# Performance work log

Measured on AMD Instinct MI355X. Metric: run time of the kernel, lower is better.

## Reference

```python
import jax, jax.numpy as jnp
import numpy as np

N_HEADS = 16


def layernorm(x, g, b, eps=1e-5):
    mu = jnp.mean(x, axis=-1, keepdims=True)
    var = jnp.var(x, axis=-1, keepdims=True)
    return (x - mu) * jax.lax.rsqrt(var + eps) * g + b


def mha(x, w_qkv, b_qkv, w_o, b_o, n_heads):
    # standard multi-head self-attention (dropout off / eval mode)
    B, S, D = x.shape
    hd = D // n_heads
    qkv = x @ w_qkv + b_qkv                      # [B,S,3D]
    q, k, v = jnp.split(qkv, 3, axis=-1)
    q = q.reshape(B, S, n_heads, hd).transpose(0, 2, 1, 3)  # bhsd
    k = k.reshape(B, S, n_heads, hd).transpose(0, 2, 1, 3)
    v = v.reshape(B, S, n_heads, hd).transpose(0, 2, 1, 3)
    att = jnp.einsum('bhqd,bhkd->bhqk', q, k) / jnp.sqrt(jnp.asarray(hd, x.dtype))
    att = jax.nn.softmax(att, axis=-1)
    out = jnp.einsum('bhqk,bhkd->bhqd', att, v)
    out = out.transpose(0, 2, 1, 3).reshape(B, S, D)
    return out @ w_o + b_o


def setup_inputs() -> dict:
    key = jax.random.key(0)
    ks = jax.random.split(key, 12)
    B, Sx, Sz, D = 4, 1024, 1024, 1024
    H = D * 4
    s = 0.02
    return {
        'x': jax.random.normal(ks[0], (B, Sx, D), jnp.float32),
        'z': jax.random.normal(ks[1], (B, Sz, D), jnp.float32),
        'g1': jnp.ones((D,), jnp.float32),
        'b1': jnp.zeros((D,), jnp.float32),
        'w_qkv': jax.random.normal(ks[2], (D, 3 * D), jnp.float32) * s,
        'b_qkv': jnp.zeros((3 * D,), jnp.float32),
        'w_o': jax.random.normal(ks[3], (D, D), jnp.float32) * s,
        'b_o': jnp.zeros((D,), jnp.float32),
        'w_kv': jax.random.normal(ks[4], (D, 2 * D), jnp.float32) * s,
        'b_kv': jnp.zeros((2 * D,), jnp.float32),
        'g2': jnp.ones((D,), jnp.float32),
        'b2': jnp.zeros((D,), jnp.float32),
        'w_m1': jax.random.normal(ks[5], (D, H), jnp.float32) * s,
        'b_m1': jnp.zeros((H,), jnp.float32),
        'w_m2': jax.random.normal(ks[6], (H, D), jnp.float32) * s,
        'b_m2': jnp.zeros((D,), jnp.float32),
    }


def reference(x, z, g1, b1, w_qkv, b_qkv, w_o, b_o, w_kv, b_kv, g2, b2, w_m1, b_m1, w_m2, b_m2):
    # q = x + self_mha(ln1(x))
    q = x + mha(layernorm(x, g1, b1), w_qkv, b_qkv, w_o, b_o, N_HEADS)
    # single-head cross attention: k,v from z, scale by sqrt(dim)
    kv = z @ w_kv + b_kv
    k, v = jnp.split(kv, 2, axis=-1)            # each [B,Sz,D]
    scale = jnp.sqrt(jnp.asarray(k.shape[-1], x.dtype))
    att = jax.nn.softmax(jnp.einsum('bqd,bkd->bqk', q, k) / scale, axis=-1)
    out = jnp.einsum('bqk,bkd->bqd', att, v)
    # out = out + mlp(ln2(out))
    h = layernorm(out, g2, b2)
    h = jax.nn.gelu(h @ w_m1 + b_m1) @ w_m2 + b_m2
    return out + h
```

## Files before the change

kernel.cpp:

```cpp
#include <hip/hip_runtime.h>
#include <cstdint>
#include <cstddef>

using u16 = unsigned short;

typedef __attribute__((ext_vector_type(4))) float f32x4;
typedef __attribute__((ext_vector_type(8))) short bf16x8;

#define DEV static __device__ __forceinline__

DEV float bf2f(u16 v) {
  union { unsigned u; float f; } x; x.u = ((unsigned)v) << 16; return x.f;
}
DEV u16 f2bf(float f) {
  union { float f; unsigned u; } x; x.f = f;
  unsigned r = x.u + 0x7fffu + ((x.u >> 16) & 1u);
  return (u16)(r >> 16);
}
DEV void gload16(const void* g, void* l) {
  __builtin_amdgcn_global_load_lds((const __attribute__((address_space(1))) void*)g,
                                   (__attribute__((address_space(3))) void*)l, 16, 0, 0);
}
DEV float fast_gelu(float x) {
  const float y = 0.7978845608028654f * (x + 0.044715f * x * x * x);
  const float e = __builtin_amdgcn_exp2f(y * 2.8853900817779268f);
  const float t = 1.0f - 2.0f * __builtin_amdgcn_rcpf(e + 1.0f);
  return 0.5f * x * (1.0f + t);
}

DEV float rowmax16_dpp(float v) {
  union { float f; int i; } a, b;
  a.f = v;
  b.i = __builtin_amdgcn_update_dpp(0, a.i, 0x121, 0xf, 0xf, true); a.f = fmaxf(a.f, b.f);
  b.i = __builtin_amdgcn_update_dpp(0, a.i, 0x122, 0xf, 0xf, true); a.f = fmaxf(a.f, b.f);
  b.i = __builtin_amdgcn_update_dpp(0, a.i, 0x124, 0xf, 0xf, true); a.f = fmaxf(a.f, b.f);
  b.i = __builtin_amdgcn_update_dpp(0, a.i, 0x128, 0xf, 0xf, true); a.f = fmaxf(a.f, b.f);
  return a.f;
}

template <typename OutT, bool GELU, int BN, bool SPLIT>
__global__ __launch_bounds__(256, 4) void gemm_nt(
    const u16* __restrict__ A, const u16* __restrict__ Bt, OutT* __restrict__ C,
    int K, int lda, int ldb, int ldc,
    const float* __restrict__ bias,
    const float* __restrict__ resF, const u16* __restrict__ resB, int ldr,
    float scale,
    long long sA, long long sB, long long sC, long long sR,
    int kSlices)
{
  constexpr int NW = (BN == 128) ? 64 : 32;
  constexpr int NJ = NW / 16;
  __shared__ u16 As[128 * 32];
  __shared__ u16 Bs[BN * 32];

  const int z = blockIdx.z;
  const int bz = z / kSlices;
  const int ks = z - bz * kSlices;
  const int Ksl = K / kSlices;
  const int kbeg = ks * Ksl, kend = kbeg + Ksl;

  A  += (size_t)bz * sA;
  Bt += (size_t)bz * sB;
  if constexpr (SPLIT) C += (size_t)ks * sC;
  else                 C += (size_t)bz * sC;
  const int m0 = blockIdx.y * 128, n0 = blockIdx.x * BN;
  const int tid = threadIdx.x;
  const int lane = tid & 63, wave = tid >> 6;
  const int wm = (wave >> 1) * 64, wn = (wave & 1) * NW;
  const int m15 = lane & 15, quad = lane >> 4;

  const u16* Ab = A + (size_t)m0 * lda;
  const u16* Bb = Bt + (size_t)n0 * ldb;
  const int r0 = tid >> 2, cc8 = (tid & 3) * 8;

  f32x4 acc[4][NJ];
#pragma unroll
  for (int i = 0; i < 4; i++)
#pragma unroll
    for (int j = 0; j < NJ; j++) acc[i][j] = (f32x4){0.f, 0.f, 0.f, 0.f};

  for (int k0 = kbeg; k0 < kend; k0 += 32) {
    __syncthreads();
    gload16(Ab + (size_t)r0 * lda + k0 + cc8,        &As[tid * 8]);
    gload16(Ab + (size_t)(r0 + 64) * lda + k0 + cc8, &As[2048 + tid * 8]);
    gload16(Bb + (size_t)r0 * ldb + k0 + cc8,        &Bs[tid * 8]);
    if constexpr (BN == 128)
      gload16(Bb + (size_t)(r0 + 64) * ldb + k0 + cc8, &Bs[2048 + tid * 8]);
    __syncthreads();
    bf16x8 af[4], bfr[NJ];
#pragma unroll
    for (int i = 0; i < 4; i++) af[i]  = *(const bf16x8*)&As[(wm + i * 16 + m15) * 32 + quad * 8];
#pragma unroll
    for (int j = 0; j < NJ; j++) bfr[j] = *(const bf16x8*)&Bs[(wn + j * 16 + m15) * 32 + quad * 8];
#pragma unroll
    for (int i = 0; i < 4; i++)
#pragma unroll
      for (int j = 0; j < NJ; j++)
        acc[i][j] = __builtin_amdgcn_mfma_f32_16x16x32_bf16(af[i], bfr[j], acc[i][j], 0, 0, 0);
  }

  const float* resFb = resF ? resF + (size_t)bz * sR : nullptr;
  const u16*   resBb = resB ? resB + (size_t)bz * sR : nullptr;

#pragma unroll
  for (int i = 0; i < 4; i++) {
    const int rowb = m0 + wm + i * 16 + quad * 4;
#pragma unroll
    for (int r = 0; r < 4; r++) {
      const size_t rowoff = (size_t)(rowb + r) * ldc;
      const size_t resoff = (size_t)(rowb + r) * ldr;
#pragma unroll
      for (int j = 0; j < NJ; j++) {
        const int col = n0 + wn + j * 16 + m15;
        float v = acc[i][j][r] * scale;
        if constexpr (SPLIT) {
          ((u16*)C)[rowoff + col] = f2bf(v);
        } else {
          if (bias) v += bias[col];
          if (GELU) v = fast_gelu(v);
          if (resFb) v += resFb[resoff + col];
          if (resBb) v += bf2f(resBb[resoff + col]);
          if constexpr (sizeof(OutT) == 4) C[rowoff + col] = v;
          else ((u16*)C)[rowoff + col] = f2bf(v);
        }
      }
    }
  }
}

__global__ __launch_bounds__(256) void mlp2_reduce_k(
    const u16* __restrict__ part, long long sliceStride,
    const u16* __restrict__ outb, const float* __restrict__ b_m2,
    float* __restrict__ outF)
{
  const size_t i = (size_t)blockIdx.x * 256 + threadIdx.x;
  const int col = (int)((i * 4) & 1023);
  const ushort4 u = ((const ushort4*)outb)[i];
  float4 o;
  o.x = bf2f(u.x) + b_m2[col + 0];
  o.y = bf2f(u.y) + b_m2[col + 1];
  o.z = bf2f(u.z) + b_m2[col + 2];
  o.w = bf2f(u.w) + b_m2[col + 3];
#pragma unroll
  for (int ks = 0; ks < 4; ks++) {
    const ushort4 p = ((const ushort4*)(part + (size_t)ks * sliceStride))[i];
    o.x += bf2f(p.x); o.y += bf2f(p.y); o.z += bf2f(p.z); o.w += bf2f(p.w);
  }
  ((float4*)outF)[i] = o;
}

__global__ __launch_bounds__(256) void transpose_all_k(
    const float* __restrict__ w_qkv, const float* __restrict__ w_o,
    const float* __restrict__ w_kv,  const float* __restrict__ w_m1,
    const float* __restrict__ w_m2,
    u16* __restrict__ wqkvT, u16* __restrict__ woT, u16* __restrict__ wkvT,
    u16* __restrict__ wm1T,  u16* __restrict__ wm2T)
{
  __shared__ u16 tile[32][33];
  int idx = blockIdx.x;
  const float* in; u16* out; int gx, ldin, ldout;
  if (idx < 3072)      { in = w_qkv; out = wqkvT; gx = 96;  ldin = 3072; ldout = 1024; }
  else if (idx < 4096) { idx -= 3072; in = w_o;  out = woT;  gx = 32;  ldin = 1024; ldout = 1024; }
  else if (idx < 6144) { idx -= 4096; in = w_kv; out = wkvT; gx = 64;  ldin = 2048; ldout = 1024; }
  else if (idx < 10240){ idx -= 6144; in = w_m1; out = wm1T; gx = 128; ldin = 4096; ldout = 1024; }
  else                 { idx -= 10240; in = w_m2; out = wm2T; gx = 32; ldin = 1024; ldout = 4096; }
  const int bx = idx % gx, by = idx / gx;
  const int tx = threadIdx.x & 31, ty = threadIdx.x >> 5;
  const int x = bx * 32 + tx;
#pragma unroll
  for (int j = 0; j < 4; j++)
    tile[ty + j * 8][tx] = f2bf(in[(size_t)(by * 32 + ty + j * 8) * ldin + x]);
  __syncthreads();
  const int x2 = by * 32 + tx;
#pragma unroll
  for (int j = 0; j < 4; j++)
    out[(size_t)(bx * 32 + ty + j * 8) * ldout + x2] = tile[tx][ty + j * 8];
}

__global__ __launch_bounds__(256) void prep_k(
    const float* __restrict__ x, const float* __restrict__ g, const float* __restrict__ bb,
    u16* __restrict__ xln, const float* __restrict__ z, u16* __restrict__ zb)
{
  const int row = blockIdx.x;
  const int t = threadIdx.x;
  if (blockIdx.y == 1) {
    const size_t i = (size_t)row * 256 + t;
    const float4 f = ((const float4*)z)[i];
    ushort4 o; o.x = f2bf(f.x); o.y = f2bf(f.y); o.z = f2bf(f.z); o.w = f2bf(f.w);
    ((ushort4*)zb)[i] = o;
    return;
  }
  float v[4];
  const float4 f = ((const float4*)(x + (size_t)row * 1024))[t];
  v[0] = f.x; v[1] = f.y; v[2] = f.z; v[3] = f.w;
  float s = v[0] + v[1] + v[2] + v[3];
  float sq = v[0]*v[0] + v[1]*v[1] + v[2]*v[2] + v[3]*v[3];
#pragma unroll
  for (int off = 1; off < 64; off <<= 1) { s += __shfl_xor(s, off); sq += __shfl_xor(sq, off); }
  __shared__ float red[8];
  const int wv = t >> 6;
  if ((t & 63) == 0) { red[wv] = s; red[4 + wv] = sq; }
  __syncthreads();
  s = red[0] + red[1] + red[2] + red[3];
  sq = red[4] + red[5] + red[6] + red[7];
  const float mean = s * (1.0f / 1024.0f);
  const float var = sq * (1.0f / 1024.0f) - mean * mean;
  const float rstd = rsqrtf(var + 1e-5f);
  const int c = t * 4;
  ushort4 o;
  o.x = f2bf((v[0] - mean) * rstd * g[c + 0] + bb[c + 0]);
  o.y = f2bf((v[1] - mean) * rstd * g[c + 1] + bb[c + 1]);
  o.z = f2bf((v[2] - mean) * rstd * g[c + 2] + bb[c + 2]);
  o.w = f2bf((v[3] - mean) * rstd * g[c + 3] + bb[c + 3]);
  ((ushort4*)(xln + (size_t)row * 1024))[t] = o;
}

__global__ __launch_bounds__(256) void transpose_v_self(
    const u16* __restrict__ qkv, u16* __restrict__ vT)
{
  __shared__ u16 tile[32][33];
  const int z = blockIdx.z, b = z >> 4, h = z & 15;
  const u16* in = qkv + (size_t)b * 1024 * 3072 + 2048 + h * 64;
  u16* out = vT + (size_t)z * 64 * 1024;
  const int tx = threadIdx.x & 31, ty = threadIdx.x >> 5;
  const int key0 = blockIdx.x * 32, d0 = blockIdx.y * 32;
#pragma unroll
  for (int j = 0; j < 4; j++)
    tile[ty + j * 8][tx] = in[(size_t)(key0 + ty + j * 8) * 3072 + d0 + tx];
  __syncthreads();
#pragma unroll
  for (int j = 0; j < 4; j++)
    out[(size_t)(d0 + ty + j * 8) * 1024 + key0 + tx] = tile[tx][ty + j * 8];
}

__global__ __launch_bounds__(256, 5) void flash_self_attn3(
    const u16* __restrict__ qkv, const u16* __restrict__ vT, u16* __restrict__ outp)
{
  __shared__ u16 Ks[64 * 72];
  __shared__ u16 Vs[64 * 72];
  __shared__ u16 Ps[4][16 * 72];
  const int b = blockIdx.z, h = blockIdx.y, q0 = blockIdx.x * 64;
  const int tid = threadIdx.x;
  const int lane = tid & 63, w = tid >> 6;
  const int m15 = lane & 15, quad = lane >> 4;
  const float L2E = 1.4426950408889634f;

  const size_t base = (size_t)b * 1024 * 3072;
  const u16* qb  = qkv + base + (size_t)q0 * 3072 + h * 64;
  const u16* kb  = qkv + base + 1024 + h * 64;
  const u16* vtb = vT + (size_t)(b * 16 + h) * 64 * 1024;

  const int r8 = tid >> 3, c8 = (tid & 7) * 8;

  bf16x8 aq[2];
#pragma unroll
  for (int kk = 0; kk < 2; kk++) {
    const bf16x8 raw = *(const bf16x8*)(qb + (size_t)(w * 16 + m15) * 3072 + kk * 32 + quad * 8);
#pragma unroll
    for (int j = 0; j < 8; j++)
      ((u16*)&aq[kk])[j] = f2bf(bf2f(((const u16*)&raw)[j]) * 0.125f);
  }

  const short oneb = (short)0x3F80;
  const bf16x8 ones = {oneb, oneb, oneb, oneb, oneb, oneb, oneb, oneb};

  float mL[4];
  f32x4 lacc;
  f32x4 oacc[4];
#pragma unroll
  for (int r = 0; r < 4; r++) mL[r] = -3.0e38f;
  lacc = (f32x4){0.f, 0.f, 0.f, 0.f};
#pragma unroll
  for (int d = 0; d < 4; d++) oacc[d] = (f32x4){0.f, 0.f, 0.f, 0.f};

  for (int kt = 0; kt < 16; kt++) {
    const int key0 = kt * 64;
    bf16x8 kreg[2], vreg[2];
#pragma unroll
    for (int i = 0; i < 2; i++) {
      kreg[i] = *(const bf16x8*)(kb + (size_t)(key0 + r8 + i * 32) * 3072 + c8);
      vreg[i] = *(const bf16x8*)(vtb + (size_t)(r8 + i * 32) * 1024 + key0 + c8);
    }
    __syncthreads();
#pragma unroll
    for (int i = 0; i < 2; i++) {
      *(bf16x8*)&Ks[(r8 + i * 32) * 72 + c8] = kreg[i];
      *(bf16x8*)&Vs[(r8 + i * 32) * 72 + c8] = vreg[i];
    }
    __syncthreads();

    f32x4 sacc[4];
#pragma unroll
    for (int n = 0; n < 4; n++) sacc[n] = (f32x4){0.f, 0.f, 0.f, 0.f};
#pragma unroll
    for (int kk = 0; kk < 2; kk++)
#pragma unroll
      for (int n = 0; n < 4; n++) {
        const bf16x8 bk = *(const bf16x8*)&Ks[(n * 16 + m15) * 72 + kk * 32 + quad * 8];
        sacc[n] = __builtin_amdgcn_mfma_f32_16x16x32_bf16(aq[kk], bk, sacc[n], 0, 0, 0);
      }

    float al[4];
#pragma unroll
    for (int r = 0; r < 4; r++) {
      float v = fmaxf(fmaxf(sacc[0][r], sacc[1][r]), fmaxf(sacc[2][r], sacc[3][r]));
      v = rowmax16_dpp(v) * L2E;
      const float mnew = fmaxf(mL[r], v);
      al[r] = __builtin_amdgcn_exp2f(mL[r] - mnew);
      mL[r] = mnew;
    }
#pragma unroll
    for (int n = 0; n < 4; n++)
#pragma unroll
      for (int r = 0; r < 4; r++) {
        const float p = __builtin_amdgcn_exp2f(fmaf(sacc[n][r], L2E, -mL[r]));
        Ps[w][(quad * 4 + r) * 72 + n * 16 + m15] = f2bf(p);
      }
#pragma unroll
    for (int r = 0; r < 4; r++) {
      lacc[r] *= al[r];
#pragma unroll
      for (int d = 0; d < 4; d++) oacc[d][r] *= al[r];
    }

    bf16x8 ap[2];
    ap[0] = *(const bf16x8*)&Ps[w][m15 * 72 + quad * 8];
    ap[1] = *(const bf16x8*)&Ps[w][m15 * 72 + 32 + quad * 8];
    lacc = __builtin_amdgcn_mfma_f32_16x16x32_bf16(ap[0], ones, lacc, 0, 0, 0);
    lacc = __builtin_amdgcn_mfma_f32_16x16x32_bf16(ap[1], ones, lacc, 0, 0, 0);
#pragma unroll
    for (int kk = 0; kk < 2; kk++)
#pragma unroll
      for (int d = 0; d < 4; d++) {
        const bf16x8 bv = *(const bf16x8*)&Vs[(d * 16 + m15) * 72 + kk * 32 + quad * 8];
        oacc[d] = __builtin_amdgcn_mfma_f32_16x16x32_bf16(ap[kk], bv, oacc[d], 0, 0, 0);
      }
  }

  u16* ob = outp + (size_t)(b * 1024 + q0 + w * 16 + quad * 4) * 1024 + h * 64 + m15;
#pragma unroll
  for (int r = 0; r < 4; r++) {
    const float inv = 1.0f / lacc[r];
#pragma unroll
    for (int d = 0; d < 4; d++)
      ob[(size_t)r * 1024 + d * 16] = f2bf(oacc[d][r] * inv);
  }
}

__global__ __launch_bounds__(256) void layernorm_b_k(
    const u16* __restrict__ x, const float* __restrict__ g, const float* __restrict__ bb,
    u16* __restrict__ y)
{
  const int row = blockIdx.x;
  const int t = threadIdx.x;
  float v[4];
  const ushort4 u = ((const ushort4*)(x + (size_t)row * 1024))[t];
  v[0] = bf2f(u.x); v[1] = bf2f(u.y); v[2] = bf2f(u.z); v[3] = bf2f(u.w);
  float s = v[0] + v[1] + v[2] + v[3];
  float sq = v[0]*v[0] + v[1]*v[1] + v[2]*v[2] + v[3]*v[3];
#pragma unroll
  for (int off = 1; off < 64; off <<= 1) { s += __shfl_xor(s, off); sq += __shfl_xor(sq, off); }
  __shared__ float red[8];
  const int wv = t >> 6;
  if ((t & 63) == 0) { red[wv] = s; red[4 + wv] = sq; }
  __syncthreads();
  s = red[0] + red[1] + red[2] + red[3];
  sq = red[4] + red[5] + red[6] + red[7];
  const float mean = s * (1.0f / 1024.0f);
  const float var = sq * (1.0f / 1024.0f) - mean * mean;
  const float rstd = rsqrtf(var + 1e-5f);
  const int c = t * 4;
  ushort4 o;
  o.x = f2bf((v[0] - mean) * rstd * g[c + 0] + bb[c + 0]);
  o.y = f2bf((v[1] - mean) * rstd * g[c + 1] + bb[c + 1]);
  o.z = f2bf((v[2] - mean) * rstd * g[c + 2] + bb[c + 2]);
  o.w = f2bf((v[3] - mean) * rstd * g[c + 3] + bb[c + 3]);
  ((ushort4*)(y + (size_t)row * 1024))[t] = o;
}

__global__ __launch_bounds__(256) void softmax_rows_k(const float* __restrict__ S, u16* __restrict__ P)
{
  const int row = blockIdx.x;
  const int t = threadIdx.x;
  const float4 f = ((const float4*)(S + (size_t)row * 1024))[t];
  float mx = fmaxf(fmaxf(f.x, f.y), fmaxf(f.z, f.w));
#pragma unroll
  for (int off = 1; off < 64; off <<= 1) mx = fmaxf(mx, __shfl_xor(mx, off));
  __shared__ float red[8];
  const int wv = t >> 6;
  if ((t & 63) == 0) red[wv] = mx;
  __syncthreads();
  mx = fmaxf(fmaxf(red[0], red[1]), fmaxf(red[2], red[3]));
  float e0 = __expf(f.x - mx), e1 = __expf(f.y - mx), e2 = __expf(f.z - mx), e3 = __expf(f.w - mx);
  float s = e0 + e1 + e2 + e3;
#pragma unroll
  for (int off = 1; off < 64; off <<= 1) s += __shfl_xor(s, off);
  if ((t & 63) == 0) red[4 + wv] = s;
  __syncthreads();
  s = red[4] + red[5] + red[6] + red[7];
  const float inv = 1.0f / s;
  ushort4 o; o.x = f2bf(e0 * inv); o.y = f2bf(e1 * inv); o.z = f2bf(e2 * inv); o.w = f2bf(e3 * inv);
  ((ushort4*)(P + (size_t)row * 1024))[t] = o;
}

__global__ __launch_bounds__(256) void transpose_k(
    const u16* __restrict__ in, u16* __restrict__ out,
    int ldin, int ldout, long long sIn, long long sOut)
{
  __shared__ u16 tile[32][33];
  in  += (size_t)blockIdx.z * sIn;
  out += (size_t)blockIdx.z * sOut;
  const int tx = threadIdx.x & 31, ty = threadIdx.x >> 5;
  const int x = blockIdx.x * 32 + tx;
#pragma unroll
  for (int j = 0; j < 4; j++)
    tile[ty + j * 8][tx] = in[(size_t)(blockIdx.y * 32 + ty + j * 8) * ldin + x];
  __syncthreads();
  const int x2 = blockIdx.y * 32 + tx;
#pragma unroll
  for (int j = 0; j < 4; j++)
    out[(size_t)(blockIdx.x * 32 + ty + j * 8) * ldout + x2] = tile[tx][ty + j * 8];
}

extern "C" void kernel_launch(void* const* d_in, const int* in_sizes, int n_in,
                              void* d_out, int out_size, void* d_ws, size_t ws_size,
                              hipStream_t stream)
{
  const float* x     = (const float*)d_in[0];
  const float* z     = (const float*)d_in[1];
  const float* g1    = (const float*)d_in[2];
  const float* b1    = (const float*)d_in[3];
  const float* w_qkv = (const float*)d_in[4];
  const float* b_qkv = (const float*)d_in[5];
  const float* w_o   = (const float*)d_in[6];
  const float* b_o   = (const float*)d_in[7];
  const float* w_kv  = (const float*)d_in[8];
  const float* b_kv  = (const float*)d_in[9];
  const float* g2    = (const float*)d_in[10];
  const float* b2    = (const float*)d_in[11];
  const float* w_m1  = (const float*)d_in[12];
  const float* b_m1  = (const float*)d_in[13];
  const float* w_m2  = (const float*)d_in[14];
  const float* b_m2  = (const float*)d_in[15];
  float* outF = (float*)d_out;

  char* ws = (char*)d_ws;
  const size_t MB = 1024ull * 1024ull;
  u16*   qkv   = (u16*)(ws + 0);
  u16*   Pm    = (u16*)(ws + 0);
  u16*   hm    = (u16*)(ws + 0);
  u16*   zb    = (u16*)(ws + 24 * MB);
  u16*   vTs   = (u16*)(ws + 24 * MB);
  u16*   xln   = (u16*)(ws + 32 * MB);
  u16*   mpart = (u16*)(ws + 32 * MB);
  u16*   qbuf  = (u16*)(ws + 40 * MB);
  u16*   kv    = (u16*)(ws + 48 * MB);
  float* Ssc   = (float*)(ws + 64 * MB);
  u16*   h1    = (u16*)(ws + 64 * MB);
  u16*   outb  = (u16*)(ws + 80 * MB);
  u16*   wqkvT = (u16*)(ws + 88 * MB);
  u16*   woT   = (u16*)(ws + 94 * MB);
  u16*   wkvT  = (u16*)(ws + 96 * MB);
  u16*   wm1T  = (u16*)(ws + 100 * MB);
  u16*   wm2T  = (u16*)(ws + 108 * MB);
  u16*   vT    = (u16*)(ws + 116 * MB);

  dim3 blk(256);
  const long long M1 = 1024 * 1024;

  hipLaunchKernelGGL(transpose_all_k, dim3(14336), blk, 0, stream,
                     w_qkv, w_o, w_kv, w_m1, w_m2, wqkvT, woT, wkvT, wm1T, wm2T);
  hipLaunchKernelGGL(prep_k, dim3(4096, 2), blk, 0, stream, x, g1, b1, xln, z, zb);

  hipLaunchKernelGGL((gemm_nt<u16, false, 128, false>), dim3(16, 32, 1), blk, 0, stream,
                     zb, wkvT, kv, 1024, 1024, 1024, 2048,
                     b_kv, (const float*)nullptr, (const u16*)nullptr, 0, 1.0f, 0LL, 0LL, 0LL, 0LL, 1);
  hipLaunchKernelGGL((gemm_nt<u16, false, 128, false>), dim3(24, 32, 1), blk, 0, stream,
                     xln, wqkvT, qkv, 1024, 1024, 1024, 3072,
                     b_qkv, (const float*)nullptr, (const u16*)nullptr, 0, 1.0f, 0LL, 0LL, 0LL, 0LL, 1);
  hipLaunchKernelGGL(transpose_v_self, dim3(32, 2, 64), blk, 0, stream, qkv, vTs);
  hipLaunchKernelGGL(flash_self_attn3, dim3(16, 16, 4), blk, 0, stream, qkv, vTs, xln);
  hipLaunchKernelGGL((gemm_nt<u16, false, 64, false>), dim3(16, 32, 1), blk, 0, stream,
                     xln, woT, qbuf, 1024, 1024, 1024, 1024,
                     b_o, x, (const u16*)nullptr, 1024, 1.0f, 0LL, 0LL, 0LL, 0LL, 1);
  hipLaunchKernelGGL((gemm_nt<float, false, 64, false>), dim3(16, 8, 4), blk, 0, stream,
                     qbuf, kv, Ssc, 1024, 1024, 2048, 1024,
                     (const float*)nullptr, (const float*)nullptr, (const u16*)nullptr, 0,
                     0.03125f, M1, 2 * M1, M1, 0LL, 1);
  hipLaunchKernelGGL(softmax_rows_k, dim3(4096), blk, 0, stream, Ssc, Pm);
  hipLaunchKernelGGL(transpose_k, dim3(32, 32, 4), blk, 0, stream,
                     kv + 1024, vT, 2048, 1024, 2 * M1, M1);
  hipLaunchKernelGGL((gemm_nt<u16, false, 64, false>), dim3(16, 8, 4), blk, 0, stream,
                     Pm, vT, outb, 1024, 1024, 1024, 1024,
                     (const float*)nullptr, (const float*)nullptr, (const u16*)nullptr, 0,
                     1.0f, M1, M1, M1, 0LL, 1);
  hipLaunchKernelGGL(layernorm_b_k, dim3(4096), blk, 0, stream, (const u16*)outb, g2, b2, h1);
  hipLaunchKernelGGL((gemm_nt<u16, true, 128, false>), dim3(32, 32, 1), blk, 0, stream,
                     h1, wm1T, hm, 1024, 1024, 1024, 4096,
                     b_m1, (const float*)nullptr, (const u16*)nullptr, 0, 1.0f, 0LL, 0LL, 0LL, 0LL, 1);
  hipLaunchKernelGGL((gemm_nt<u16, false, 128, true>), dim3(8, 32, 4), blk, 0, stream,
                     hm, wm2T, mpart, 4096, 4096, 4096, 1024,
                     (const float*)nullptr, (const float*)nullptr, (const u16*)nullptr, 0,
                     1.0f, 0LL, 0LL, 4LL * M1, 0LL, 4);
  hipLaunchKernelGGL(mlp2_reduce_k, dim3(4096), blk, 0, stream,
                     mpart, 4LL * M1, outb, b_m2, outF);
}
```

Measured before the change: 502.6 us.

## Double GEMM K-step, merge QKV/KV GEMMs, fuse prep and softmax/transpose launches

The GEMM body now stages 64 K-elements per barrier pair in two 32-wide halves, doubling shared memory per block and halving syncs. The QKV and KV projections are merged into one dual-dispatch launch. Weight transposes are combined with layernorm/z conversion, and softmax with the V transpose, to cut launch count and tail idle time. Larger LDS use may reduce occupancy under the 4-block launch bound.

```diff
diff --git a/kernel.cpp b/kernel.cpp
--- a/kernel.cpp
+++ b/kernel.cpp
@@ -39,21 +39,19 @@
 }
 
 template <typename OutT, bool GELU, int BN, bool SPLIT>
-__global__ __launch_bounds__(256, 4) void gemm_nt(
+DEV void gemm_body(
     const u16* __restrict__ A, const u16* __restrict__ Bt, OutT* __restrict__ C,
     int K, int lda, int ldb, int ldc,
     const float* __restrict__ bias,
     const float* __restrict__ resF, const u16* __restrict__ resB, int ldr,
-    float scale,
-    long long sA, long long sB, long long sC, long long sR,
-    int kSlices)
+    float scale, long long sA, long long sB, long long sC, long long sR,
+    int kSlices, int bx, int by, int z,
+    u16* As , u16* Bs )
 {
   constexpr int NW = (BN == 128) ? 64 : 32;
   constexpr int NJ = NW / 16;
-  __shared__ u16 As[128 * 32];
-  __shared__ u16 Bs[BN * 32];
-
-  const int z = blockIdx.z;
+  constexpr int BH = BN * 32;
+
   const int bz = z / kSlices;
   const int ks = z - bz * kSlices;
   const int Ksl = K / kSlices;
@@ -63,7 +61,7 @@
   Bt += (size_t)bz * sB;
   if constexpr (SPLIT) C += (size_t)ks * sC;
   else                 C += (size_t)bz * sC;
-  const int m0 = blockIdx.y * 128, n0 = blockIdx.x * BN;
+  const int m0 = by * 128, n0 = bx * BN;
   const int tid = threadIdx.x;
   const int lane = tid & 63, wave = tid >> 6;
   const int wm = (wave >> 1) * 64, wn = (wave & 1) * NW;
@@ -79,24 +77,35 @@
 #pragma unroll
     for (int j = 0; j < NJ; j++) acc[i][j] = (f32x4){0.f, 0.f, 0.f, 0.f};
 
-  for (int k0 = kbeg; k0 < kend; k0 += 32) {
+  for (int k0 = kbeg; k0 < kend; k0 += 64) {
     __syncthreads();
-    gload16(Ab + (size_t)r0 * lda + k0 + cc8,        &As[tid * 8]);
-    gload16(Ab + (size_t)(r0 + 64) * lda + k0 + cc8, &As[2048 + tid * 8]);
-    gload16(Bb + (size_t)r0 * ldb + k0 + cc8,        &Bs[tid * 8]);
-    if constexpr (BN == 128)
-      gload16(Bb + (size_t)(r0 + 64) * ldb + k0 + cc8, &Bs[2048 + tid * 8]);
+#pragma unroll
+    for (int h = 0; h < 2; h++) {
+      const int kc = k0 + h * 32 + cc8;
+      u16* Ah = As + h * 4096;
+      gload16(Ab + (size_t)r0 * lda + kc,        Ah + tid * 8);
+      gload16(Ab + (size_t)(r0 + 64) * lda + kc, Ah + 2048 + tid * 8);
+      u16* Bh = Bs + h * BH;
+      gload16(Bb + (size_t)r0 * ldb + kc,        Bh + tid * 8);
+      if constexpr (BN == 128)
+        gload16(Bb + (size_t)(r0 + 64) * ldb + kc, Bh + 2048 + tid * 8);
+    }
     __syncthreads();
-    bf16x8 af[4], bfr[NJ];
-#pragma unroll
-    for (int i = 0; i < 4; i++) af[i]  = *(const bf16x8*)&As[(wm + i * 16 + m15) * 32 + quad * 8];
-#pragma unroll
-    for (int j = 0; j < NJ; j++) bfr[j] = *(const bf16x8*)&Bs[(wn + j * 16 + m15) * 32 + quad * 8];
-#pragma unroll
-    for (int i = 0; i < 4; i++)
+#pragma unroll
+    for (int h = 0; h < 2; h++) {
+      bf16x8 af[4], bfr[NJ];
+#pragma unroll
+      for (int i = 0; i < 4; i++)
+        af[i] = *(const bf16x8*)&As[h * 4096 + (wm + i * 16 + m15) * 32 + quad * 8];
 #pragma unroll
       for (int j = 0; j < NJ; j++)
-        acc[i][j] = __builtin_amdgcn_mfma_f32_16x16x32_bf16(af[i], bfr[j], acc[i][j], 0, 0, 0);
+        bfr[j] = *(const bf16x8*)&Bs[h * BH + (wn + j * 16 + m15) * 32 + quad * 8];
+#pragma unroll
+      for (int i = 0; i < 4; i++)
+#pragma unroll
+        for (int j = 0; j < NJ; j++)
+          acc[i][j] = __builtin_amdgcn_mfma_f32_16x16x32_bf16(af[i], bfr[j], acc[i][j], 0, 0, 0);
+    }
   }
 
   const float* resFb = resF ? resF + (size_t)bz * sR : nullptr;
@@ -128,6 +137,41 @@
   }
 }
 
+template <typename OutT, bool GELU, int BN, bool SPLIT>
+__global__ __launch_bounds__(256, 4) void gemm_nt(
+    const u16* __restrict__ A, const u16* __restrict__ Bt, OutT* __restrict__ C,
+    int K, int lda, int ldb, int ldc,
+    const float* __restrict__ bias,
+    const float* __restrict__ resF, const u16* __restrict__ resB, int ldr,
+    float scale, long long sA, long long sB, long long sC, long long sR,
+    int kSlices)
+{
+  __shared__ u16 As[128 * 64];
+  __shared__ u16 Bs[BN * 64];
+  gemm_body<OutT, GELU, BN, SPLIT>(A, Bt, C, K, lda, ldb, ldc, bias, resF, resB,
+                                   ldr, scale, sA, sB, sC, sR, kSlices,
+                                   blockIdx.x, blockIdx.y, blockIdx.z, As, Bs);
+}
+
+__global__ __launch_bounds__(256, 4) void gemm_dual(
+    const u16* __restrict__ A1, const u16* __restrict__ B1, u16* __restrict__ C1,
+    int ldc1, const float* __restrict__ bias1, int nx1,
+    const u16* __restrict__ A2, const u16* __restrict__ B2, u16* __restrict__ C2,
+    int ldc2, const float* __restrict__ bias2)
+{
+  __shared__ u16 As[128 * 64];
+  __shared__ u16 Bs[128 * 64];
+  const int bx = blockIdx.x;
+  if (bx < nx1)
+    gemm_body<u16, false, 128, false>(A1, B1, C1, 1024, 1024, 1024, ldc1, bias1,
+                                      nullptr, nullptr, 0, 1.0f, 0, 0, 0, 0, 1,
+                                      bx, blockIdx.y, 0, As, Bs);
+  else
+    gemm_body<u16, false, 128, false>(A2, B2, C2, 1024, 1024, 1024, ldc2, bias2,
+                                      nullptr, nullptr, 0, 1.0f, 0, 0, 0, 0, 1,
+                                      bx - nx1, blockIdx.y, 0, As, Bs);
+}
+
 __global__ __launch_bounds__(256) void mlp2_reduce_k(
     const u16* __restrict__ part, long long sliceStride,
     const u16* __restrict__ outb, const float* __restrict__ b_m2,
@@ -149,15 +193,54 @@
   ((float4*)outF)[i] = o;
 }
 
-__global__ __launch_bounds__(256) void transpose_all_k(
+__global__ __launch_bounds__(256) void prep_all_k(
     const float* __restrict__ w_qkv, const float* __restrict__ w_o,
     const float* __restrict__ w_kv,  const float* __restrict__ w_m1,
     const float* __restrict__ w_m2,
     u16* __restrict__ wqkvT, u16* __restrict__ woT, u16* __restrict__ wkvT,
-    u16* __restrict__ wm1T,  u16* __restrict__ wm2T)
+    u16* __restrict__ wm1T,  u16* __restrict__ wm2T,
+    const float* __restrict__ x, const float* __restrict__ g1,
+    const float* __restrict__ b1, u16* __restrict__ xln,
+    const float* __restrict__ z, u16* __restrict__ zb)
 {
   __shared__ u16 tile[32][33];
+  __shared__ float red[8];
   int idx = blockIdx.x;
+  const int t = threadIdx.x;
+  if (idx >= 14336) {
+    idx -= 14336;
+    if (idx >= 4096) {
+      const size_t i = (size_t)(idx - 4096) * 256 + t;
+      const float4 f = ((const float4*)z)[i];
+      ushort4 o; o.x = f2bf(f.x); o.y = f2bf(f.y); o.z = f2bf(f.z); o.w = f2bf(f.w);
+      ((ushort4*)zb)[i] = o;
+      return;
+    }
+    const int row = idx;
+    float v[4];
+    const float4 f = ((const float4*)(x + (size_t)row * 1024))[t];
+    v[0] = f.x; v[1] = f.y; v[2] = f.z; v[3] = f.w;
+    float s = v[0] + v[1] + v[2] + v[3];
+    float sq = v[0]*v[0] + v[1]*v[1] + v[2]*v[2] + v[3]*v[3];
+#pragma unroll
+    for (int off = 1; off < 64; off <<= 1) { s += __shfl_xor(s, off); sq += __shfl_xor(sq, off); }
+    const int wv = t >> 6;
+    if ((t & 63) == 0) { red[wv] = s; red[4 + wv] = sq; }
+    __syncthreads();
+    s = red[0] + red[1] + red[2] + red[3];
+    sq = red[4] + red[5] + red[6] + red[7];
+    const float mean = s * (1.0f / 1024.0f);
+    const float var = sq * (1.0f / 1024.0f) - mean * mean;
+    const float rstd = rsqrtf(var + 1e-5f);
+    const int c = t * 4;
+    ushort4 o;
+    o.x = f2bf((v[0] - mean) * rstd * g1[c + 0] + b1[c + 0]);
+    o.y = f2bf((v[1] - mean) * rstd * g1[c + 1] + b1[c + 1]);
+    o.z = f2bf((v[2] - mean) * rstd * g1[c + 2] + b1[c + 2]);
+    o.w = f2bf((v[3] - mean) * rstd * g1[c + 3] + b1[c + 3]);
+    ((ushort4*)(xln + (size_t)row * 1024))[t] = o;
+    return;
+  }
   const float* in; u16* out; int gx, ldin, ldout;
   if (idx < 3072)      { in = w_qkv; out = wqkvT; gx = 96;  ldin = 3072; ldout = 1024; }
   else if (idx < 4096) { idx -= 3072; in = w_o;  out = woT;  gx = 32;  ldin = 1024; ldout = 1024; }
@@ -165,54 +248,16 @@
   else if (idx < 10240){ idx -= 6144; in = w_m1; out = wm1T; gx = 128; ldin = 4096; ldout = 1024; }
   else                 { idx -= 10240; in = w_m2; out = wm2T; gx = 32; ldin = 1024; ldout = 4096; }
   const int bx = idx % gx, by = idx / gx;
-  const int tx = threadIdx.x & 31, ty = threadIdx.x >> 5;
-  const int x = bx * 32 + tx;
+  const int tx = t & 31, ty = t >> 5;
+  const int xx = bx * 32 + tx;
 #pragma unroll
   for (int j = 0; j < 4; j++)
-    tile[ty + j * 8][tx] = f2bf(in[(size_t)(by * 32 + ty + j * 8) * ldin + x]);
+    tile[ty + j * 8][tx] = f2bf(in[(size_t)(by * 32 + ty + j * 8) * ldin + xx]);
   __syncthreads();
   const int x2 = by * 32 + tx;
 #pragma unroll
   for (int j = 0; j < 4; j++)
     out[(size_t)(bx * 32 + ty + j * 8) * ldout + x2] = tile[tx][ty + j * 8];
-}
-
-__global__ __launch_bounds__(256) void prep_k(
-    const float* __restrict__ x, const float* __restrict__ g, const float* __restrict__ bb,
-    u16* __restrict__ xln, const float* __restrict__ z, u16* __restrict__ zb)
-{
-  const int row = blockIdx.x;
-  const int t = threadIdx.x;
-  if (blockIdx.y == 1) {
-    const size_t i = (size_t)row * 256 + t;
-    const float4 f = ((const float4*)z)[i];
-    ushort4 o; o.x = f2bf(f.x); o.y = f2bf(f.y); o.z = f2bf(f.z); o.w = f2bf(f.w);
-    ((ushort4*)zb)[i] = o;
-    return;
-  }
-  float v[4];
-  const float4 f = ((const float4*)(x + (size_t)row * 1024))[t];
-  v[0] = f.x; v[1] = f.y; v[2] = f.z; v[3] = f.w;
-  float s = v[0] + v[1] + v[2] + v[3];
-  float sq = v[0]*v[0] + v[1]*v[1] + v[2]*v[2] + v[3]*v[3];
-#pragma unroll
-  for (int off = 1; off < 64; off <<= 1) { s += __shfl_xor(s, off); sq += __shfl_xor(sq, off); }
-  __shared__ float red[8];
-  const int wv = t >> 6;
-  if ((t & 63) == 0) { red[wv] = s; red[4 + wv] = sq; }
-  __syncthreads();
-  s = red[0] + red[1] + red[2] + red[3];
-  sq = red[4] + red[5] + red[6] + red[7];
-  const float mean = s * (1.0f / 1024.0f);
-  const float var = sq * (1.0f / 1024.0f) - mean * mean;
-  const float rstd = rsqrtf(var + 1e-5f);
-  const int c = t * 4;
-  ushort4 o;
-  o.x = f2bf((v[0] - mean) * rstd * g[c + 0] + bb[c + 0]);
-  o.y = f2bf((v[1] - mean) * rstd * g[c + 1] + bb[c + 1]);
-  o.z = f2bf((v[2] - mean) * rstd * g[c + 2] + bb[c + 2]);
-  o.w = f2bf((v[3] - mean) * rstd * g[c + 3] + bb[c + 3]);
-  ((ushort4*)(xln + (size_t)row * 1024))[t] = o;
 }
 
 __global__ __launch_bounds__(256) void transpose_v_self(
@@ -378,15 +423,36 @@
   ((ushort4*)(y + (size_t)row * 1024))[t] = o;
 }
 
-__global__ __launch_bounds__(256) void softmax_rows_k(const float* __restrict__ S, u16* __restrict__ P)
-{
-  const int row = blockIdx.x;
+__global__ __launch_bounds__(256) void softmax_vt_k(
+    const float* __restrict__ S, u16* __restrict__ P,
+    const u16* __restrict__ kv, u16* __restrict__ vT)
+{
+  __shared__ u16 tile[32][33];
+  __shared__ float red[8];
   const int t = threadIdx.x;
+  int idx = blockIdx.x;
+  if (idx >= 4096) {
+    idx -= 4096;
+    const int bx = idx & 31, by = (idx >> 5) & 31, bz = idx >> 10;
+    const u16* in = kv + 1024 + (size_t)bz * 2097152;
+    u16* out = vT + (size_t)bz * 1048576;
+    const int tx = t & 31, ty = t >> 5;
+    const int x = bx * 32 + tx;
+#pragma unroll
+    for (int j = 0; j < 4; j++)
+      tile[ty + j * 8][tx] = in[(size_t)(by * 32 + ty + j * 8) * 2048 + x];
+    __syncthreads();
+    const int x2 = by * 32 + tx;
+#pragma unroll
+    for (int j = 0; j < 4; j++)
+      out[(size_t)(bx * 32 + ty + j * 8) * 1024 + x2] = tile[tx][ty + j * 8];
+    return;
+  }
+  const int row = idx;
   const float4 f = ((const float4*)(S + (size_t)row * 1024))[t];
   float mx = fmaxf(fmaxf(f.x, f.y), fmaxf(f.z, f.w));
 #pragma unroll
   for (int off = 1; off < 64; off <<= 1) mx = fmaxf(mx, __shfl_xor(mx, off));
-  __shared__ float red[8];
   const int wv = t >> 6;
   if ((t & 63) == 0) red[wv] = mx;
   __syncthreads();
@@ -401,25 +467,6 @@
   const float inv = 1.0f / s;
   ushort4 o; o.x = f2bf(e0 * inv); o.y = f2bf(e1 * inv); o.z = f2bf(e2 * inv); o.w = f2bf(e3 * inv);
   ((ushort4*)(P + (size_t)row * 1024))[t] = o;
-}
-
-__global__ __launch_bounds__(256) void transpose_k(
-    const u16* __restrict__ in, u16* __restrict__ out,
-    int ldin, int ldout, long long sIn, long long sOut)
-{
-  __shared__ u16 tile[32][33];
-  in  += (size_t)blockIdx.z * sIn;
-  out += (size_t)blockIdx.z * sOut;
-  const int tx = threadIdx.x & 31, ty = threadIdx.x >> 5;
-  const int x = blockIdx.x * 32 + tx;
-#pragma unroll
-  for (int j = 0; j < 4; j++)
-    tile[ty + j * 8][tx] = in[(size_t)(blockIdx.y * 32 + ty + j * 8) * ldin + x];
-  __syncthreads();
-  const int x2 = blockIdx.y * 32 + tx;
-#pragma unroll
-  for (int j = 0; j < 4; j++)
-    out[(size_t)(blockIdx.x * 32 + ty + j * 8) * ldout + x2] = tile[tx][ty + j * 8];
 }
 
 extern "C" void kernel_launch(void* const* d_in, const int* in_sizes, int n_in,
@@ -468,16 +515,12 @@
   dim3 blk(256);
   const long long M1 = 1024 * 1024;
 
-  hipLaunchKernelGGL(transpose_all_k, dim3(14336), blk, 0, stream,
-                     w_qkv, w_o, w_kv, w_m1, w_m2, wqkvT, woT, wkvT, wm1T, wm2T);
-  hipLaunchKernelGGL(prep_k, dim3(4096, 2), blk, 0, stream, x, g1, b1, xln, z, zb);
-
-  hipLaunchKernelGGL((gemm_nt<u16, false, 128, false>), dim3(16, 32, 1), blk, 0, stream,
-                     zb, wkvT, kv, 1024, 1024, 1024, 2048,
-                     b_kv, (const float*)nullptr, (const u16*)nullptr, 0, 1.0f, 0LL, 0LL, 0LL, 0LL, 1);
-  hipLaunchKernelGGL((gemm_nt<u16, false, 128, false>), dim3(24, 32, 1), blk, 0, stream,
-                     xln, wqkvT, qkv, 1024, 1024, 1024, 3072,
-                     b_qkv, (const float*)nullptr, (const u16*)nullptr, 0, 1.0f, 0LL, 0LL, 0LL, 0LL, 1);
+  hipLaunchKernelGGL(prep_all_k, dim3(22528), blk, 0, stream,
+                     w_qkv, w_o, w_kv, w_m1, w_m2, wqkvT, woT, wkvT, wm1T, wm2T,
+                     x, g1, b1, xln, z, zb);
+  hipLaunchKernelGGL(gemm_dual, dim3(40, 32, 1), blk, 0, stream,
+                     xln, wqkvT, qkv, 3072, b_qkv, 24,
+                     zb, wkvT, kv, 2048, b_kv);
   hipLaunchKernelGGL(transpose_v_self, dim3(32, 2, 64), blk, 0, stream, qkv, vTs);
   hipLaunchKernelGGL(flash_self_attn3, dim3(16, 16, 4), blk, 0, stream, qkv, vTs, xln);
   hipLaunchKernelGGL((gemm_nt<u16, false, 64, false>), dim3(16, 32, 1), blk, 0, stream,
@@ -487,9 +530,7 @@
                      qbuf, kv, Ssc, 1024, 1024, 2048, 1024,
                      (const float*)nullptr, (const float*)nullptr, (const u16*)nullptr, 0,
                      0.03125f, M1, 2 * M1, M1, 0LL, 1);
-  hipLaunchKernelGGL(softmax_rows_k, dim3(4096), blk, 0, stream, Ssc, Pm);
-  hipLaunchKernelGGL(transpose_k, dim3(32, 32, 4), blk, 0, stream,
-                     kv + 1024, vT, 2048, 1024, 2 * M1, M1);
+  hipLaunchKernelGGL(softmax_vt_k, dim3(8192), blk, 0, stream, Ssc, Pm, kv, vT);
   hipLaunchKernelGGL((gemm_nt<u16, false, 64, false>), dim3(16, 8, 4), blk, 0, stream,
                      Pm, vT, outb, 1024, 1024, 1024, 1024,
                      (const float*)nullptr, (const float*)nullptr, (const u16*)nullptr, 0,
```

After: 463.9 us. 1.08x faster.
